# Optimization experiments

Measured on AMD Instinct MI355X. Metric: run time of the kernel, lower is better.

## Reference

```python
import jax, jax.numpy as jnp
import numpy as np

STRIDE, PAD, DIL = 1, 1, 1


def setup_inputs() -> dict:
    key = jax.random.key(0)
    k1, k2, k3, k4, k5 = jax.random.split(key, 5)
    N, Cin, H, W = 8, 256, 64, 64
    Cout, K = 256, 3
    x = jax.random.normal(k1, (N, Cin, H, W), dtype=jnp.float32)
    offset = jax.random.normal(k2, (N, 2 * K * K, H, W), dtype=jnp.float32)
    mask = jax.random.uniform(k3, (N, K * K, H, W), dtype=jnp.float32)
    weight = jax.random.normal(k4, (Cout, Cin, K, K), dtype=jnp.float32) * 0.02
    bias = jax.random.normal(k5, (Cout,), dtype=jnp.float32)
    return {"x": x, "offset": offset, "mask": mask, "weight": weight, "bias": bias}


def _gather(im_flat, idx):
    # im_flat: (N, Goff, Cg, H*W); idx: (N, Goff, KK, Ho, Wo) int32
    # -> (N, Goff, Cg, KK, Ho, Wo)
    f = lambda imf, ix: imf[:, ix]
    return jax.vmap(jax.vmap(f))(im_flat, idx)


def _deform_conv2d(x, offset, mask, weight, bias):
    N, Cin, H, W = x.shape
    Cout, Cin_g, Kh, Kw = weight.shape
    KK = Kh * Kw
    Goff = offset.shape[1] // (2 * KK)
    Ho = (H + 2 * PAD - (DIL * (Kh - 1) + 1)) // STRIDE + 1
    Wo = (W + 2 * PAD - (DIL * (Kw - 1) + 1)) // STRIDE + 1

    # base sampling grid per kernel tap: (KK, Ho, Wo)
    py = (jnp.arange(Kh)[:, None] * DIL + jnp.arange(Ho)[None, :] * STRIDE - PAD).astype(jnp.float32)
    px = (jnp.arange(Kw)[:, None] * DIL + jnp.arange(Wo)[None, :] * STRIDE - PAD).astype(jnp.float32)
    y_base = jnp.broadcast_to(py[:, None, :, None], (Kh, Kw, Ho, Wo)).reshape(KK, Ho, Wo)
    x_base = jnp.broadcast_to(px[None, :, None, :], (Kh, Kw, Ho, Wo)).reshape(KK, Ho, Wo)

    off = offset.reshape(N, Goff, KK, 2, Ho, Wo)  # [...,0]=dy, [...,1]=dx
    ys = y_base[None, None] + off[:, :, :, 0]  # (N, Goff, KK, Ho, Wo)
    xs = x_base[None, None] + off[:, :, :, 1]

    Cg = Cin // Goff
    im_flat = x.reshape(N, Goff, Cg, H * W)

    y0 = jnp.floor(ys)
    x0 = jnp.floor(xs)
    acc = jnp.zeros((N, Goff, Cg, KK, Ho, Wo), dtype=x.dtype)
    for dy in (0.0, 1.0):
        for dx in (0.0, 1.0):
            yi = y0 + dy
            xi = x0 + dx
            wgt = (1.0 - jnp.abs(ys - yi)) * (1.0 - jnp.abs(xs - xi))
            valid = (yi >= 0) & (yi < H) & (xi >= 0) & (xi < W)
            idx = (jnp.clip(yi, 0, H - 1) * W + jnp.clip(xi, 0, W - 1)).astype(jnp.int32)
            g = _gather(im_flat, idx)  # (N,Goff,Cg,KK,Ho,Wo)
            acc = acc + g * (wgt * valid.astype(x.dtype))[:, :, None]

    m = mask.reshape(N, Goff, KK, Ho, Wo)
    sampled = acc * m[:, :, None]  # DCNv2 modulation

    # grouped conv accumulate as GEMM over (Cin_g*KK)
    gw = Cin // Cin_g
    cols = sampled.reshape(N, gw, Cin_g * KK, Ho * Wo)
    wflat = weight.reshape(gw, Cout // gw, Cin_g * KK)
    out = jnp.einsum('goc,ngcl->ngol', wflat, cols).reshape(N, Cout, Ho, Wo)
    return out + bias[None, :, None, None]


def reference(x, offset, mask, weight, bias):
    return _deform_conv2d(x, offset, mask, weight, bias)
```

## Files before the change

kernel.cpp:

```cpp
#include <hip/hip_runtime.h>
#include <stdint.h>

typedef unsigned int u32;
typedef unsigned short u16;
typedef float f32x4 __attribute__((ext_vector_type(4)));
typedef __fp16 h16x2 __attribute__((ext_vector_type(2)));
typedef _Float16 f16x8 __attribute__((ext_vector_type(8)));
typedef float f4u __attribute__((ext_vector_type(4), aligned(4)));

#define NB   8
#define CIN  256
#define HH   64
#define WW   64
#define HW   4096
#define COUT 256
#define BSTR 264

__device__ __forceinline__ u32 pkh(float lo, float hi) {
  h16x2 h = __builtin_amdgcn_cvt_pkrtz(lo, hi);
  return __builtin_bit_cast(u32, h);
}
union HU { u32 u; h16x2 h; };

__global__ __launch_bounds__(256) void prep_all(const float* __restrict__ x,
                                                const float* __restrict__ wgt,
                                                u32* __restrict__ xT,
                                                u32* __restrict__ W2f32) {
  int b = blockIdx.x;
  int t = threadIdx.x;
  if (b < 512) {
    __shared__ u32 tile[64][129];
    int n = b >> 6, hw0 = (b & 63) << 6;
    int hw4 = (t & 15) << 2;
    int cp0 = t >> 4;
    const float* xb = x + (size_t)n * CIN * HW + hw0 + hw4;
#pragma unroll
    for (int it = 0; it < 8; ++it) {
      int cp = (it << 4) + cp0;
      int c = cp << 1;
      f4u v0 = *(const f4u*)(xb + (size_t)c * HW);
      f4u v1 = *(const f4u*)(xb + (size_t)(c + 1) * HW);
      tile[hw4 + 0][cp] = pkh(v0.x, v1.x);
      tile[hw4 + 1][cp] = pkh(v0.y, v1.y);
      tile[hw4 + 2][cp] = pkh(v0.z, v1.z);
      tile[hw4 + 3][cp] = pkh(v0.w, v1.w);
    }
    __syncthreads();
    u32* outp = xT + ((size_t)(n * HW + hw0)) * 128;
    int cp = t & 127, hb = t >> 7;
#pragma unroll
    for (int it = 0; it < 32; ++it) {
      int hwl = (it << 1) + hb;
      outp[(size_t)hwl * 128 + cp] = tile[hwl][cp];
    }
  } else {
    int tt = (b - 512) * 256 + t;
    int cp = tt & 127, co = tt >> 7;
    int c = cp << 1;
    const float* p = wgt + ((size_t)co * CIN + c) * 9;
    f4u q0 = *(const f4u*)(p + 0);
    f4u q1 = *(const f4u*)(p + 4);
    f4u q2 = *(const f4u*)(p + 8);
    f4u q3 = *(const f4u*)(p + 12);
    float e16 = p[16], e17 = p[17];
    float a0[9], a1[9];
    a0[0]=q0.x; a0[1]=q0.y; a0[2]=q0.z; a0[3]=q0.w;
    a0[4]=q1.x; a0[5]=q1.y; a0[6]=q1.z; a0[7]=q1.w; a0[8]=q2.x;
    a1[0]=q2.y; a1[1]=q2.z; a1[2]=q2.w;
    a1[3]=q3.x; a1[4]=q3.y; a1[5]=q3.z; a1[6]=q3.w; a1[7]=e16; a1[8]=e17;
    int cc = c >> 5;
    int j = (c >> 1) & 3;
    int lane = (co & 15) | (((c >> 3) & 3) << 4);
    int tile_ = ((co >> 6) << 2) | ((co >> 4) & 3);
#pragma unroll
    for (int kk = 0; kk < 9; ++kk) {
      int frag = (kk * 8 + cc) * 16 + tile_;
      W2f32[(size_t)frag * 256 + lane * 4 + j] = pkh(a0[kk], a1[kk]);
    }
  }
}

__global__ __launch_bounds__(512, 4) void dcn_main(
    const float* __restrict__ offset, const float* __restrict__ mask,
    const float* __restrict__ bias, const u16* __restrict__ xT,
    const u16* __restrict__ W2f, float* __restrict__ out) {
  __shared__ __align__(16) u16 Bs[2][64 * BSTR];
  __shared__ __align__(8)  uint2 swl[576];
  __shared__ __align__(8)  ushort4 sol[576];

  int bid = blockIdx.x;
  int n = bid & 7;
  int ho = bid >> 3;
  int t = threadIdx.x;
  int lane = t & 63;
  int w = t >> 6;

  for (int i = t; i < 576; i += 512) {
    int kk = i >> 6, p = i & 63;
    int ky = kk / 3, kx = kk - ky * 3;
    int sp = (ho << 6) + p;
    float dy = offset[(((size_t)n * 18 + kk * 2 + 0) << 12) + sp];
    float dx = offset[(((size_t)n * 18 + kk * 2 + 1) << 12) + sp];
    float m  = mask  [(((size_t)n * 9  + kk) << 12) + sp];
    float ys = (float)(ky + ho - 1) + dy;
    float xs = (float)(kx + p  - 1) + dx;
    float y0f = floorf(ys), x0f = floorf(xs);
    float fy = ys - y0f, fx = xs - x0f;
    int y0 = (int)y0f, x0 = (int)x0f;
    int y1 = y0 + 1, x1 = x0 + 1;
    float vy0 = (y0 >= 0 && y0 < HH) ? 1.f : 0.f;
    float vy1 = (y1 >= 0 && y1 < HH) ? 1.f : 0.f;
    float vx0 = (x0 >= 0 && x0 < WW) ? 1.f : 0.f;
    float vx1 = (x1 >= 0 && x1 < WW) ? 1.f : 0.f;
    float w0 = (1.f - fy) * (1.f - fx) * m * vy0 * vx0;
    float w1 = (1.f - fy) * fx * m * vy0 * vx1;
    float w2 = fy * (1.f - fx) * m * vy1 * vx0;
    float w3 = fy * fx * m * vy1 * vx1;
    int iy0 = min(max(y0, 0), HH - 1), iy1 = min(max(y1, 0), HH - 1);
    int ix0 = min(max(x0, 0), WW - 1), ix1 = min(max(x1, 0), WW - 1);
    ushort4 pv;
    pv.x = (u16)((iy0 << 6) + ix0);
    pv.y = (u16)((iy0 << 6) + ix1);
    pv.z = (u16)((iy1 << 6) + ix0);
    pv.w = (u16)((iy1 << 6) + ix1);
    swl[i] = make_uint2(pkh(w0, w1), pkh(w2, w3));
    sol[i] = pv;
  }
  __syncthreads();

  f32x4 acc[2][4];
#pragma unroll
  for (int a = 0; a < 2; ++a)
#pragma unroll
    for (int b2 = 0; b2 < 4; ++b2) acc[a][b2] = {0.f, 0.f, 0.f, 0.f};

  const char* xTn = (const char*)xT + ((size_t)n * HW << 9);
  int ml = lane & 15, q = lane >> 4;
  int hwid = t >> 5;
  int l32 = t & 31;
  int tile0 = ((w >> 1) << 2) + ((w & 1) << 1);
  const char* bch = xTn + (l32 << 4);

#define CMB(G, WT) do {                                                \
    float wt = (WT);                                                   \
    HU h0, h1, h2, h3;                                                 \
    h0.u = (G).x; h1.u = (G).y; h2.u = (G).z; h3.u = (G).w;            \
    s0 = __builtin_fmaf((float)h0.h.x, wt, s0);                        \
    s1 = __builtin_fmaf((float)h0.h.y, wt, s1);                        \
    s2 = __builtin_fmaf((float)h1.h.x, wt, s2);                        \
    s3 = __builtin_fmaf((float)h1.h.y, wt, s3);                        \
    s4 = __builtin_fmaf((float)h2.h.x, wt, s4);                        \
    s5 = __builtin_fmaf((float)h2.h.y, wt, s5);                        \
    s6 = __builtin_fmaf((float)h3.h.x, wt, s6);                        \
    s7 = __builtin_fmaf((float)h3.h.y, wt, s7);                        \
  } while (0)

  auto build0 = [&](int i) {
    int px = (i << 4) + hwid;
    uint2 wu = swl[px];
    ushort4 pv = sol[px];
    HU ha, hb; ha.u = wu.x; hb.u = wu.y;
    uint4 G0 = *(const uint4*)(bch + ((int)pv.x << 9));
    uint4 G1 = *(const uint4*)(bch + ((int)pv.y << 9));
    uint4 G2 = *(const uint4*)(bch + ((int)pv.z << 9));
    uint4 G3 = *(const uint4*)(bch + ((int)pv.w << 9));
    float s0=0.f,s1=0.f,s2=0.f,s3=0.f,s4=0.f,s5=0.f,s6=0.f,s7=0.f;
    CMB(G0, (float)ha.h.x);
    CMB(G1, (float)ha.h.y);
    CMB(G2, (float)hb.h.x);
    CMB(G3, (float)hb.h.y);
    uint4 pkd;
    pkd.x = pkh(s0, s1); pkd.y = pkh(s2, s3);
    pkd.z = pkh(s4, s5); pkd.w = pkh(s6, s7);
    *(uint4*)((char*)&Bs[0][0] + px * (BSTR * 2) + (l32 << 4)) = pkd;
  };

  auto af_load = [&](int fidx, int mt) {
    return *(const f16x8*)(W2f +
           (((size_t)((fidx << 4) + tile0 + mt)) << 9) + (lane << 3));
  };

#pragma unroll
  for (int i = 0; i < 4; ++i) build0(i);
  __syncthreads();

  f16x8 afc0 = af_load(0, 0);
  f16x8 afc1 = af_load(0, 1);

#pragma unroll 1
  for (int kk = 0; kk < 9; ++kk) {
    int cur = kk & 1;
    char* Bw = (char*)&Bs[cur ^ 1][0];
    const char* Br = (const char*)&Bs[cur][0];
    int fbase = kk << 3;
#pragma unroll
    for (int g = 0; g < 4; ++g) {
      int px = (g << 4) + hwid;
      uint4 G0, G1, G2, G3;
      float cw0, cw1, cw2, cw3;
      if (kk < 8) {
        int ii = ((kk + 1) << 6) + px;
        uint2 wu = swl[ii];
        ushort4 pv = sol[ii];
        HU ha, hb; ha.u = wu.x; hb.u = wu.y;
        cw0 = (float)ha.h.x; cw1 = (float)ha.h.y;
        cw2 = (float)hb.h.x; cw3 = (float)hb.h.y;
        G0 = *(const uint4*)(bch + ((int)pv.x << 9));
        G1 = *(const uint4*)(bch + ((int)pv.y << 9));
        G2 = *(const uint4*)(bch + ((int)pv.z << 9));
        G3 = *(const uint4*)(bch + ((int)pv.w << 9));
      }
#pragma unroll
      for (int c2 = 0; c2 < 2; ++c2) {
        int cc = (g << 1) | c2;
        int nf = fbase + cc + 1; if (nf > 71) nf = 71;
        f16x8 afn0 = af_load(nf, 0);
        f16x8 afn1 = af_load(nf, 1);
        f16x8 bf[4];
#pragma unroll
        for (int nt = 0; nt < 4; ++nt)
          bf[nt] = *(const f16x8*)(Br + ((nt << 4) + ml) * (BSTR * 2) +
                                   (cc << 6) + (q << 4));
#pragma unroll
        for (int nt = 0; nt < 4; ++nt)
          acc[0][nt] = __builtin_amdgcn_mfma_f32_16x16x32_f16(afc0, bf[nt],
                                                              acc[0][nt], 0, 0, 0);
#pragma unroll
        for (int nt = 0; nt < 4; ++nt)
          acc[1][nt] = __builtin_amdgcn_mfma_f32_16x16x32_f16(afc1, bf[nt],
                                                              acc[1][nt], 0, 0, 0);
        afc0 = afn0; afc1 = afn1;
      }
      if (kk < 8) {
        float s0=0.f,s1=0.f,s2=0.f,s3=0.f,s4=0.f,s5=0.f,s6=0.f,s7=0.f;
        CMB(G0, cw0);
        CMB(G1, cw1);
        CMB(G2, cw2);
        CMB(G3, cw3);
        uint4 pkd;
        pkd.x = pkh(s0, s1); pkd.y = pkh(s2, s3);
        pkd.z = pkh(s4, s5); pkd.w = pkh(s6, s7);
        *(uint4*)(Bw + px * (BSTR * 2) + (l32 << 4)) = pkd;
      }
    }
    __syncthreads();
  }

  size_t obase = ((size_t)n * COUT) * HW + ((size_t)ho << 6);
#pragma unroll
  for (int mt = 0; mt < 2; ++mt) {
#pragma unroll
    for (int r = 0; r < 4; ++r) {
      int co = (w << 5) + (mt << 4) + (q << 2) + r;
      float bv = bias[co];
#pragma unroll
      for (int nt = 0; nt < 4; ++nt) {
        int wo = (nt << 4) + ml;
        out[obase + (size_t)co * HW + wo] = acc[mt][nt][r] + bv;
      }
    }
  }
}

extern "C" void kernel_launch(void* const* d_in, const int* in_sizes, int n_in,
                              void* d_out, int out_size, void* d_ws, size_t ws_size,
                              hipStream_t stream) {
  const float* x      = (const float*)d_in[0];
  const float* offset = (const float*)d_in[1];
  const float* mask   = (const float*)d_in[2];
  const float* weight = (const float*)d_in[3];
  const float* bias   = (const float*)d_in[4];
  float* out = (float*)d_out;

  u16* xT  = (u16*)d_ws;
  u16* W2f = (u16*)((char*)d_ws + (size_t)NB * HW * CIN * 2);

  prep_all<<<640, 256, 0, stream>>>(x, weight, (u32*)xT, (u32*)W2f);
  dcn_main<<<512, 512, 0, stream>>>(offset, mask, bias, xT, W2f, out);
}
```

Measured before the change: 144.6 us.

## Process two output rows per block with split-K waves and LDS reduction

Each block now covers 128 pixels (two output rows) using 1024 threads, halving the grid to 256 blocks. Waves are split into two groups that each handle half of the input-channel chunks per tap (split-K), and the partial accumulators are reduced through LDS before the bias add and store. The intent is to reuse each weight fragment across twice as many pixels and to raise MFMA work per barrier. In exchange, a block needs more LDS and an extra reduction pass, the A-fragment prefetch is dropped, and 256 blocks may underfill the device's compute units.

```diff
diff --git a/kernel.cpp b/kernel.cpp
--- a/kernel.cpp
+++ b/kernel.cpp
@@ -14,6 +14,7 @@
 #define WW   64
 #define HW   4096
 #define COUT 256
+#define NPX  128
 #define BSTR 264
 
 __device__ __forceinline__ u32 pkh(float lo, float hi) {
@@ -80,30 +81,31 @@
   }
 }
 
-__global__ __launch_bounds__(512, 4) void dcn_main(
+__global__ __launch_bounds__(1024, 4) void dcn_main(
     const float* __restrict__ offset, const float* __restrict__ mask,
     const float* __restrict__ bias, const u16* __restrict__ xT,
     const u16* __restrict__ W2f, float* __restrict__ out) {
-  __shared__ __align__(16) u16 Bs[2][64 * BSTR];
-  __shared__ __align__(8)  uint2 swl[576];
-  __shared__ __align__(8)  ushort4 sol[576];
+  __shared__ __align__(16) u16 Bs[2][NPX * BSTR];
+  __shared__ __align__(8)  uint2 swl[1152];
+  __shared__ __align__(8)  ushort4 sol[1152];
 
   int bid = blockIdx.x;
   int n = bid & 7;
-  int ho = bid >> 3;
+  int hp = bid >> 3;
   int t = threadIdx.x;
   int lane = t & 63;
   int w = t >> 6;
 
-  for (int i = t; i < 576; i += 512) {
-    int kk = i >> 6, p = i & 63;
+  for (int i = t; i < 1152; i += 1024) {
+    int kk = i >> 7, p = i & 127;
     int ky = kk / 3, kx = kk - ky * 3;
-    int sp = (ho << 6) + p;
+    int sp = (hp << 7) + p;
+    int ho = (hp << 1) + (p >> 6);
     float dy = offset[(((size_t)n * 18 + kk * 2 + 0) << 12) + sp];
     float dx = offset[(((size_t)n * 18 + kk * 2 + 1) << 12) + sp];
     float m  = mask  [(((size_t)n * 9  + kk) << 12) + sp];
     float ys = (float)(ky + ho - 1) + dy;
-    float xs = (float)(kx + p  - 1) + dx;
+    float xs = (float)(kx + (p & 63) - 1) + dx;
     float y0f = floorf(ys), x0f = floorf(xs);
     float fy = ys - y0f, fx = xs - x0f;
     int y0 = (int)y0f, x0 = (int)x0f;
@@ -128,17 +130,18 @@
   }
   __syncthreads();
 
-  f32x4 acc[2][4];
+  f32x4 acc[2][8];
 #pragma unroll
   for (int a = 0; a < 2; ++a)
 #pragma unroll
-    for (int b2 = 0; b2 < 4; ++b2) acc[a][b2] = {0.f, 0.f, 0.f, 0.f};
+    for (int b2 = 0; b2 < 8; ++b2) acc[a][b2] = {0.f, 0.f, 0.f, 0.f};
 
   const char* xTn = (const char*)xT + ((size_t)n * HW << 9);
   int ml = lane & 15, q = lane >> 4;
-  int hwid = t >> 5;
+  int hw32 = t >> 5;
   int l32 = t & 31;
-  int tile0 = ((w >> 1) << 2) + ((w & 1) << 1);
+  int strip = w & 7, pr = w >> 3;
+  int tile0 = ((strip >> 1) << 2) + ((strip & 1) << 1);
   const char* bch = xTn + (l32 << 4);
 
 #define CMB(G, WT) do {                                                \
@@ -155,8 +158,8 @@
     s7 = __builtin_fmaf((float)h3.h.y, wt, s7);                        \
   } while (0)
 
-  auto build0 = [&](int i) {
-    int px = (i << 4) + hwid;
+  auto build0 = [&](int g) {
+    int px = (g << 5) + hw32;
     uint2 wu = swl[px];
     ushort4 pv = sol[px];
     HU ha, hb; ha.u = wu.x; hb.u = wu.y;
@@ -176,16 +179,13 @@
   };
 
   auto af_load = [&](int fidx, int mt) {
-    return *(const f16x8*)(W2f +
-           (((size_t)((fidx << 4) + tile0 + mt)) << 9) + (lane << 3));
+    return *(const f16x8*)(W2f + (((size_t)((fidx << 4) + tile0 + mt)) << 9) +
+                           (lane << 3));
   };
 
 #pragma unroll
-  for (int i = 0; i < 4; ++i) build0(i);
+  for (int g = 0; g < 4; ++g) build0(g);
   __syncthreads();
-
-  f16x8 afc0 = af_load(0, 0);
-  f16x8 afc1 = af_load(0, 1);
 
 #pragma unroll 1
   for (int kk = 0; kk < 9; ++kk) {
@@ -195,48 +195,45 @@
     int fbase = kk << 3;
 #pragma unroll
     for (int g = 0; g < 4; ++g) {
-      int px = (g << 4) + hwid;
+      int px = (g << 5) + hw32;
       uint4 G0, G1, G2, G3;
-      float cw0, cw1, cw2, cw3;
       if (kk < 8) {
-        int ii = ((kk + 1) << 6) + px;
-        uint2 wu = swl[ii];
-        ushort4 pv = sol[ii];
-        HU ha, hb; ha.u = wu.x; hb.u = wu.y;
-        cw0 = (float)ha.h.x; cw1 = (float)ha.h.y;
-        cw2 = (float)hb.h.x; cw3 = (float)hb.h.y;
+        ushort4 pv = sol[((kk + 1) << 7) + px];
         G0 = *(const uint4*)(bch + ((int)pv.x << 9));
         G1 = *(const uint4*)(bch + ((int)pv.y << 9));
         G2 = *(const uint4*)(bch + ((int)pv.z << 9));
         G3 = *(const uint4*)(bch + ((int)pv.w << 9));
       }
-#pragma unroll
-      for (int c2 = 0; c2 < 2; ++c2) {
-        int cc = (g << 1) | c2;
-        int nf = fbase + cc + 1; if (nf > 71) nf = 71;
-        f16x8 afn0 = af_load(nf, 0);
-        f16x8 afn1 = af_load(nf, 1);
+      {
+        int cc = (g << 1) | pr;
+        f16x8 af0 = af_load(fbase + cc, 0);
+        f16x8 af1 = af_load(fbase + cc, 1);
         f16x8 bf[4];
 #pragma unroll
-        for (int nt = 0; nt < 4; ++nt)
-          bf[nt] = *(const f16x8*)(Br + ((nt << 4) + ml) * (BSTR * 2) +
-                                   (cc << 6) + (q << 4));
-#pragma unroll
-        for (int nt = 0; nt < 4; ++nt)
-          acc[0][nt] = __builtin_amdgcn_mfma_f32_16x16x32_f16(afc0, bf[nt],
-                                                              acc[0][nt], 0, 0, 0);
-#pragma unroll
-        for (int nt = 0; nt < 4; ++nt)
-          acc[1][nt] = __builtin_amdgcn_mfma_f32_16x16x32_f16(afc1, bf[nt],
-                                                              acc[1][nt], 0, 0, 0);
-        afc0 = afn0; afc1 = afn1;
+        for (int half = 0; half < 2; ++half) {
+#pragma unroll
+          for (int j = 0; j < 4; ++j)
+            bf[j] = *(const f16x8*)(Br +
+                    ((((half << 2) + j) << 4) + ml) * (BSTR * 2) +
+                    (cc << 6) + (q << 4));
+#pragma unroll
+          for (int j = 0; j < 4; ++j)
+            acc[0][(half << 2) + j] = __builtin_amdgcn_mfma_f32_16x16x32_f16(
+                af0, bf[j], acc[0][(half << 2) + j], 0, 0, 0);
+#pragma unroll
+          for (int j = 0; j < 4; ++j)
+            acc[1][(half << 2) + j] = __builtin_amdgcn_mfma_f32_16x16x32_f16(
+                af1, bf[j], acc[1][(half << 2) + j], 0, 0, 0);
+        }
       }
       if (kk < 8) {
+        uint2 wu = swl[((kk + 1) << 7) + px];
+        HU ha, hb; ha.u = wu.x; hb.u = wu.y;
         float s0=0.f,s1=0.f,s2=0.f,s3=0.f,s4=0.f,s5=0.f,s6=0.f,s7=0.f;
-        CMB(G0, cw0);
-        CMB(G1, cw1);
-        CMB(G2, cw2);
-        CMB(G3, cw3);
+        CMB(G0, (float)ha.h.x);
+        CMB(G1, (float)ha.h.y);
+        CMB(G2, (float)hb.h.x);
+        CMB(G3, (float)hb.h.y);
         uint4 pkd;
         pkd.x = pkh(s0, s1); pkd.y = pkh(s2, s3);
         pkd.z = pkh(s4, s5); pkd.w = pkh(s6, s7);
@@ -246,17 +243,32 @@
     __syncthreads();
   }
 
-  size_t obase = ((size_t)n * COUT) * HW + ((size_t)ho << 6);
-#pragma unroll
-  for (int mt = 0; mt < 2; ++mt) {
-#pragma unroll
-    for (int r = 0; r < 4; ++r) {
-      int co = (w << 5) + (mt << 4) + (q << 2) + r;
-      float bv = bias[co];
-#pragma unroll
-      for (int nt = 0; nt < 4; ++nt) {
-        int wo = (nt << 4) + ml;
-        out[obase + (size_t)co * HW + wo] = acc[mt][nt][r] + bv;
+  float* PS = (float*)&Bs[0][0];
+  float* P = PS + strip * 4224 + lane * 66;
+  if (pr) {
+#pragma unroll
+    for (int mt = 0; mt < 2; ++mt)
+#pragma unroll
+      for (int nt = 0; nt < 8; ++nt)
+#pragma unroll
+        for (int r = 0; r < 4; ++r)
+          P[((mt << 3) + nt) * 4 + r] = acc[mt][nt][r];
+  }
+  __syncthreads();
+  if (!pr) {
+    size_t ob = (size_t)n * COUT * HW + ((size_t)hp << 7);
+#pragma unroll
+    for (int mt = 0; mt < 2; ++mt) {
+#pragma unroll
+      for (int r = 0; r < 4; ++r) {
+        int co = (strip << 5) + (mt << 4) + (q << 2) + r;
+        float bv = bias[co];
+#pragma unroll
+        for (int nt = 0; nt < 8; ++nt) {
+          int px = (nt << 4) + ml;
+          out[ob + (size_t)co * HW + px] =
+              acc[mt][nt][r] + P[((mt << 3) + nt) * 4 + r] + bv;
+        }
       }
     }
   }
@@ -276,5 +288,5 @@
   u16* W2f = (u16*)((char*)d_ws + (size_t)NB * HW * CIN * 2);
 
   prep_all<<<640, 256, 0, stream>>>(x, weight, (u32*)xT, (u32*)W2f);
-  dcn_main<<<512, 512, 0, stream>>>(offset, mask, bias, xT, W2f, out);
-}
+  dcn_main<<<256, 1024, 0, stream>>>(offset, mask, bias, xT, W2f, out);
+}
```

After: 143.7 us. About the same (-0.6%).
